# Optimization experiments

Measured on AMD Instinct MI355X. Metric: run time of the kernel, lower is better.

Reference implementation:

```python
import jax, jax.numpy as jnp
import numpy as np

N_NODES = 100000
N_EDGES = 600000
N_GRAPHS = 4096
F_IN = 74
H = 128
L = 3
BN_EPS = 1e-5


def setup_inputs() -> dict:
    key = jax.random.key(0)
    ks = jax.random.split(key, 12)
    x = jax.random.normal(ks[0], (N_NODES, F_IN), dtype=jnp.float32)
    edge_index = jax.random.randint(ks[1], (2, N_EDGES), 0, N_NODES)
    batch = jnp.sort(jax.random.randint(ks[2], (N_NODES,), 0, N_GRAPHS))

    def lin(k, fan_in, fan_out):
        return (jax.random.normal(k, (fan_in, fan_out), dtype=jnp.float32)
                / np.float32(np.sqrt(fan_in)))

    emb_W = lin(ks[3], F_IN, H)
    emb_b = jnp.zeros((H,), jnp.float32)
    conv_W = jax.random.normal(ks[4], (L, H, H), dtype=jnp.float32) / np.float32(np.sqrt(H))
    conv_b = jnp.zeros((L, H), jnp.float32)
    bn_gamma = jnp.ones((L, H), jnp.float32)
    bn_beta = jnp.zeros((L, H), jnp.float32)
    w1 = lin(ks[5], 2 * H, H)
    b1 = jnp.zeros((H,), jnp.float32)
    w2 = lin(ks[6], H, H // 2)
    b2 = jnp.zeros((H // 2,), jnp.float32)
    w3 = lin(ks[7], H // 2, 1)
    b3 = jnp.zeros((1,), jnp.float32)
    return dict(x=x, edge_index=edge_index, batch=batch,
                emb_W=emb_W, emb_b=emb_b, conv_W=conv_W, conv_b=conv_b,
                bn_gamma=bn_gamma, bn_beta=bn_beta,
                w1=w1, b1=b1, w2=w2, b2=b2, w3=w3, b3=b3)


def reference(x, edge_index, batch, emb_W, emb_b, conv_W, conv_b,
              bn_gamma, bn_beta, w1, b1, w2, b2, w3, b3):
    N = x.shape[0]
    # GCN normalization with self-loops (PyG GCNConv semantics)
    loops = jnp.arange(N)
    src = jnp.concatenate([edge_index[0], loops])  # [E+N]
    dst = jnp.concatenate([edge_index[1], loops])
    deg = jax.ops.segment_sum(jnp.ones_like(dst, jnp.float32), dst, num_segments=N)
    dinv = jax.lax.rsqrt(jnp.maximum(deg, 1.0))  # deg >= 1 due to self-loops
    norm = dinv[src] * dinv[dst]                 # [E+N]

    h = jax.nn.relu(x @ emb_W + emb_b)           # [N, H]
    for i in range(L):
        hw = h @ conv_W[i]                       # [N, H]
        msg = hw[src] * norm[:, None]            # gather + scale  [E+N, H]
        h = jax.ops.segment_sum(msg, dst, num_segments=N) + conv_b[i]
        # BatchNorm1d, training-mode batch statistics (biased variance)
        mu = jnp.mean(h, axis=0)
        var = jnp.mean((h - mu) ** 2, axis=0)
        h = (h - mu) * jax.lax.rsqrt(var + BN_EPS) * bn_gamma[i] + bn_beta[i]
        h = jax.nn.relu(h)
        # dropout: identity (inference / deterministic baseline)

    # segment mean / max pooling over graphs
    cnt = jax.ops.segment_sum(jnp.ones((N,), jnp.float32), batch, num_segments=N_GRAPHS)
    g_mean = jax.ops.segment_sum(h, batch, num_segments=N_GRAPHS) / jnp.maximum(cnt, 1.0)[:, None]
    g_max = jax.ops.segment_max(h, batch, num_segments=N_GRAPHS)
    g_max = jnp.where(jnp.isfinite(g_max), g_max, 0.0)  # guard empty segments
    g = jnp.concatenate([g_mean, g_max], axis=1)         # [G, 2H]

    h1 = jax.nn.relu(g @ w1 + b1)
    h2 = jax.nn.relu(h1 @ w2 + b2)
    return h2 @ w3 + b3                                   # [G, 1]
```

## Files before the change

### kernel.cpp

```cpp
#include <hip/hip_runtime.h>

#define NN 100000
#define NE 600000
#define NG 4096
#define FIN 74
#define HD 128
#define NL 3
#define BN_EPS 1e-5f
#define NSCAN 391
#define NHISTB 2344
#define NT16 6250
#define NSHADOW 8

typedef __attribute__((ext_vector_type(8))) short short8;
typedef __attribute__((ext_vector_type(4))) float floatx4;
typedef __attribute__((ext_vector_type(8))) unsigned short bf16x8;
typedef __attribute__((ext_vector_type(4))) unsigned short bf16x4;

__device__ __forceinline__ unsigned short f2bf(float f) {
    unsigned u = __float_as_uint(f);
    u += 0x7fff + ((u >> 16) & 1);
    return (unsigned short)(u >> 16);
}
__device__ __forceinline__ float bf2f(unsigned short u) {
    return __uint_as_float(((unsigned)u) << 16);
}

__global__ __launch_bounds__(256) void k_pre(const int* __restrict__ dst,
                                             int* __restrict__ degi,
                                             const int* __restrict__ batch,
                                             int* __restrict__ gstart,
                                             const float* __restrict__ embW,
                                             const float* __restrict__ convW,
                                             unsigned short* __restrict__ WfE,
                                             unsigned short* __restrict__ WfC) {
    int blk = blockIdx.x;
    int t = threadIdx.x;
    if (blk < NHISTB) {
        int e = blk * 256 + t;
        if (e < NE) atomicAdd(&degi[dst[e]], 1);
    } else if (blk < NHISTB + NSCAN) {
        int n = (blk - NHISTB) * 256 + t;
        if (n >= NN) return;
        int b = batch[n];
        int bp = (n == 0) ? -1 : batch[n - 1];
        for (int g = bp + 1; g <= b; g++) gstart[g] = n;
        if (n == NN - 1)
            for (int g = b + 1; g <= NG; g++) gstart[g] = NN;
    } else {
        int d = (blk - NHISTB - NSCAN) * 256 + t;
        if (d < 12288) {
            int inner = d & 511, outer = d >> 9;
            int kstep = outer % 3, nt = outer / 3;
            int g = inner >> 7, n = (inner >> 3) & 15, j = inner & 7;
            int k = kstep * 32 + g * 8 + j;
            float v = (k < FIN) ? embW[k * HD + nt * 16 + n] : 0.0f;
            WfE[d] = f2bf(v);
        } else {
            int e = d - 12288;
            if (e >= NL * 16384) return;
            int layer = e >> 14, r = e & 16383;
            int j = r & 7, n = (r >> 3) & 15, g = (r >> 7) & 3, kstep = (r >> 9) & 3, nt = r >> 11;
            int k = kstep * 32 + g * 8 + j;
            WfC[e] = f2bf(convW[layer * 16384 + k * HD + nt * 16 + n]);
        }
    }
}

__global__ __launch_bounds__(256) void k_scan1(const int* __restrict__ degi,
                                               int* __restrict__ part) {
    __shared__ int s[256];
    int t = threadIdx.x;
    int idx = blockIdx.x * 256 + t;
    s[t] = (idx < NN) ? degi[idx] : 0;
    __syncthreads();
    for (int off = 128; off > 0; off >>= 1) {
        if (t < off) s[t] += s[t + off];
        __syncthreads();
    }
    if (t == 0) part[blockIdx.x] = s[0];
}

__global__ __launch_bounds__(512) void k_scan2(int* __restrict__ part) {
    __shared__ int s[512];
    int t = threadIdx.x;
    s[t] = (t < NSCAN) ? part[t] : 0;
    __syncthreads();
    for (int off = 1; off < 512; off <<= 1) {
        int v = s[t];
        int a = (t >= off) ? s[t - off] : 0;
        __syncthreads();
        s[t] = v + a;
        __syncthreads();
    }
    if (t < NSCAN) part[t] = (t > 0) ? s[t - 1] : 0;
}

__global__ __launch_bounds__(256) void k_scan3(const int* __restrict__ degi,
                                               const int* __restrict__ part,
                                               int* __restrict__ rowptr,
                                               float* __restrict__ dinv) {
    __shared__ int s[256];
    int t = threadIdx.x;
    int idx = blockIdx.x * 256 + t;
    int v = (idx < NN) ? degi[idx] : 0;
    s[t] = v;
    __syncthreads();
    for (int off = 1; off < 256; off <<= 1) {
        int x = s[t];
        int a = (t >= off) ? s[t - off] : 0;
        __syncthreads();
        s[t] = x + a;
        __syncthreads();
    }
    if (idx < NN) {
        rowptr[idx] = part[blockIdx.x] + (s[t] - v);
        dinv[idx] = rsqrtf((float)v + 1.0f);
    }
    if (idx == 0) rowptr[NN] = NE;
}

__global__ __launch_bounds__(256) void k_fill(const int* __restrict__ src,
                                              const int* __restrict__ dst,
                                              const int* __restrict__ rowptr,
                                              int* __restrict__ cursor,
                                              int* __restrict__ col) {
    int e = blockIdx.x * 256 + threadIdx.x;
    if (e >= NE) return;
    int d = dst[e];
    int pos = rowptr[d] + atomicAdd(&cursor[d], 1);
    col[pos] = src[e];
}

__global__ __launch_bounds__(256) void k_emb(const float* __restrict__ x,
                                             const unsigned short* __restrict__ Wf,
                                             const float* __restrict__ b,
                                             const float* __restrict__ dinv,
                                             unsigned short* __restrict__ hA) {
    __shared__ __align__(16) unsigned short As[4224];
    __shared__ float dinvs[32];
    int t = threadIdx.x;
    int n0 = blockIdx.x * 32;
    if (t < 32) dinvs[t] = dinv[n0 + t];
    for (int f = t; f < 3072; f += 256) {
        int m = f / 96, kp = f % 96;
        float v = (kp < FIN) ? x[(n0 + m) * FIN + kp] : 0.0f;
        int kstep = kp >> 5, g = (kp >> 3) & 3, j = kp & 7;
        As[(kstep * 4 + g) * 264 + m * 8 + j] = f2bf(v);
    }
    __syncthreads();
    int lane = t & 63, wv = t >> 6;
    int lanelo = lane & 15, g = lane >> 4;
    floatx4 acc[2][2] = {};
#pragma unroll
    for (int kstep = 0; kstep < 3; kstep++) {
        short8 a0 = *(const short8*)&As[(kstep * 4 + g) * 264 + lanelo * 8];
        short8 a1 = *(const short8*)&As[(kstep * 4 + g) * 264 + 128 + lanelo * 8];
        short8 b0 = *(const short8*)&Wf[(((wv * 2 + 0) * 3 + kstep) * 4 + g) * 128 + lanelo * 8];
        short8 b1 = *(const short8*)&Wf[(((wv * 2 + 1) * 3 + kstep) * 4 + g) * 128 + lanelo * 8];
        acc[0][0] = __builtin_amdgcn_mfma_f32_16x16x32_bf16(a0, b0, acc[0][0], 0, 0, 0);
        acc[0][1] = __builtin_amdgcn_mfma_f32_16x16x32_bf16(a0, b1, acc[0][1], 0, 0, 0);
        acc[1][0] = __builtin_amdgcn_mfma_f32_16x16x32_bf16(a1, b0, acc[1][0], 0, 0, 0);
        acc[1][1] = __builtin_amdgcn_mfma_f32_16x16x32_bf16(a1, b1, acc[1][1], 0, 0, 0);
    }
    __syncthreads();
#pragma unroll
    for (int ns = 0; ns < 2; ns++) {
        int colc = wv * 32 + ns * 16 + lanelo;
        float bias = b[colc];
#pragma unroll
        for (int ms = 0; ms < 2; ms++)
#pragma unroll
            for (int r = 0; r < 4; r++) {
                int rowl = ms * 16 + g * 4 + r;
                As[rowl * 132 + colc] = f2bf(dinvs[rowl] * fmaxf(acc[ms][ns][r] + bias, 0.0f));
            }
    }
    __syncthreads();
#pragma unroll
    for (int i = 0; i < 2; i++) {
        int f = t * 8 + i * 2048;
        int m = f >> 7, c = f & 127;
        bf16x4 lo = *(const bf16x4*)&As[m * 132 + c];
        bf16x4 hi = *(const bf16x4*)&As[m * 132 + c + 4];
        bf16x8 o = {lo.x, lo.y, lo.z, lo.w, hi.x, hi.y, hi.z, hi.w};
        *(bf16x8*)&hA[n0 * HD + f] = o;
    }
}

__global__ __launch_bounds__(256) void k_bnact(const unsigned short* __restrict__ hpre,
                                               const float* __restrict__ bnsum,
                                               const float* __restrict__ gamma,
                                               const float* __restrict__ beta,
                                               const float* __restrict__ dinv,
                                               unsigned short* __restrict__ P) {
    int t = threadIdx.x;
    int cg = t & 15, c0 = cg * 8;
    const float inv_n = 1.0f / (float)NN;
    float sc[8], sh[8];
#pragma unroll
    for (int jj = 0; jj < 8; jj++) {
        int c = c0 + jj;
        float s = 0.0f, q = 0.0f;
#pragma unroll
        for (int kk = 0; kk < NSHADOW; kk++) {
            s += bnsum[kk * 256 + c];
            q += bnsum[kk * 256 + 128 + c];
        }
        float mu = s * inv_n;
        float var = q * inv_n - mu * mu;
        float g = gamma[c] * rsqrtf(var + BN_EPS);
        sc[jj] = g;
        sh[jj] = beta[c] - mu * g;
    }
    for (int n = blockIdx.x * 16 + (t >> 4); n < NN; n += gridDim.x * 16) {
        float d = dinv[n];
        bf16x8 u = *(const bf16x8*)&hpre[n * HD + c0];
        bf16x8 o;
#pragma unroll
        for (int i = 0; i < 8; i++)
            o[i] = f2bf(d * fmaxf(bf2f(u[i]) * sc[i] + sh[i], 0.0f));
        *(bf16x8*)&P[n * HD + c0] = o;
    }
}

__global__ __launch_bounds__(256, 8) void k_fused(const unsigned short* __restrict__ Ain,
                                                  const int* __restrict__ rowptr,
                                                  const int* __restrict__ col,
                                                  const float* __restrict__ dinv,
                                                  const unsigned short* __restrict__ Wf,
                                                  const float* __restrict__ bias,
                                                  float* __restrict__ bnout,
                                                  unsigned short* __restrict__ Aout) {
    __shared__ __align__(16) unsigned short As[2176];
    int t = threadIdx.x;
    int slot = t >> 4;
    int lanec = t & 15;
    int k0 = lanec * 8;

    int lane = t & 63, wv = t >> 6;
    int lanelo = lane & 15, g = lane >> 4;
    float bias0 = bias[wv * 32 + lanelo];
    float bias1 = bias[wv * 32 + 16 + lanelo];
    float ssum[2] = {}, ssq[2] = {};

    int n0 = blockIdx.x * 16;
    {
        int n = n0 + slot;
        float dn = dinv[n];
        float acc[8];
        bf16x8 u = *(const bf16x8*)&Ain[n * HD + k0];
#pragma unroll
        for (int i = 0; i < 8; i++) acc[i] = bf2f(u[i]);
        int j = rowptr[n], j1 = rowptr[n + 1];
        for (; j + 3 < j1; j += 4) {
            int s0 = col[j], s1 = col[j + 1], s2 = col[j + 2], s3 = col[j + 3];
            bf16x8 v0 = *(const bf16x8*)&Ain[s0 * HD + k0];
            bf16x8 v1 = *(const bf16x8*)&Ain[s1 * HD + k0];
            bf16x8 v2 = *(const bf16x8*)&Ain[s2 * HD + k0];
            bf16x8 v3 = *(const bf16x8*)&Ain[s3 * HD + k0];
#pragma unroll
            for (int i = 0; i < 8; i++) {
                float a01 = bf2f(v0[i]) + bf2f(v1[i]);
                float a23 = bf2f(v2[i]) + bf2f(v3[i]);
                acc[i] += a01 + a23;
            }
        }
        for (; j < j1; j++) {
            int s0 = col[j];
            bf16x8 v0 = *(const bf16x8*)&Ain[s0 * HD + k0];
#pragma unroll
            for (int i = 0; i < 8; i++) acc[i] += bf2f(v0[i]);
        }
        bf16x8 o;
#pragma unroll
        for (int i = 0; i < 8; i++) o[i] = f2bf(acc[i] * dn);
        *(bf16x8*)&As[lanec * 136 + slot * 8] = o;
    }
    __syncthreads();
    floatx4 macc[2] = {};
#pragma unroll
    for (int ks = 0; ks < 4; ks++) {
        short8 a = *(const short8*)&As[(ks * 4 + g) * 136 + lanelo * 8];
        short8 b0 = *(const short8*)&Wf[(((wv * 2 + 0) * 4 + ks) * 4 + g) * 128 + lanelo * 8];
        short8 b1 = *(const short8*)&Wf[(((wv * 2 + 1) * 4 + ks) * 4 + g) * 128 + lanelo * 8];
        macc[0] = __builtin_amdgcn_mfma_f32_16x16x32_bf16(a, b0, macc[0], 0, 0, 0);
        macc[1] = __builtin_amdgcn_mfma_f32_16x16x32_bf16(a, b1, macc[1], 0, 0, 0);
    }
    __syncthreads();
#pragma unroll
    for (int ns = 0; ns < 2; ns++) {
        int colc = wv * 32 + ns * 16 + lanelo;
        float bb = ns ? bias1 : bias0;
#pragma unroll
        for (int r = 0; r < 4; r++) {
            int rowl = g * 4 + r;
            float v = macc[ns][r] + bb;
            ssum[ns] += v;
            ssq[ns] += v * v;
            As[rowl * 132 + colc] = f2bf(v);
        }
    }
    __syncthreads();
    {
        int m = t >> 4, c = (t & 15) * 8;
        bf16x4 lo = *(const bf16x4*)&As[m * 132 + c];
        bf16x4 hi = *(const bf16x4*)&As[m * 132 + c + 4];
        bf16x8 o = {lo.x, lo.y, lo.z, lo.w, hi.x, hi.y, hi.z, hi.w};
        *(bf16x8*)&Aout[n0 * HD + t * 8] = o;
    }
    __syncthreads();
    float* ls = (float*)As;
    ls[t] = 0.0f;
    __syncthreads();
    {
        int colc0 = wv * 32 + lanelo;
        atomicAdd(&ls[colc0], ssum[0]);
        atomicAdd(&ls[128 + colc0], ssq[0]);
        atomicAdd(&ls[colc0 + 16], ssum[1]);
        atomicAdd(&ls[128 + colc0 + 16], ssq[1]);
    }
    __syncthreads();
    atomicAdd(&bnout[(blockIdx.x & (NSHADOW - 1)) * 256 + t], ls[t]);
}

__global__ __launch_bounds__(128) void k_pool_g(const unsigned short* __restrict__ h,
                                                const float* __restrict__ bnsum,
                                                const float* __restrict__ gamma,
                                                const float* __restrict__ beta,
                                                const int* __restrict__ gstart,
                                                float* __restrict__ gfeat) {
    int g = blockIdx.x;
    int c = threadIdx.x;
    int n0 = gstart[g], n1 = gstart[g + 1];
    const float inv_n = 1.0f / (float)NN;
    float s0 = 0.0f, q0 = 0.0f;
#pragma unroll
    for (int k = 0; k < NSHADOW; k++) {
        s0 += bnsum[k * 256 + c];
        q0 += bnsum[k * 256 + 128 + c];
    }
    float mu = s0 * inv_n;
    float var = q0 * inv_n - mu * mu;
    float sc = gamma[c] * rsqrtf(var + BN_EPS);
    float sh = beta[c] - mu * sc;
    float s = 0.0f, mx = 0.0f;
    for (int n = n0; n < n1; n++) {
        float v = fmaxf(bf2f(h[n * HD + c]) * sc + sh, 0.0f);
        s += v;
        mx = fmaxf(mx, v);
    }
    float cntf = (float)(n1 - n0);
    gfeat[g * 256 + c] = s / fmaxf(cntf, 1.0f);
    gfeat[g * 256 + HD + c] = mx;
}

__global__ __launch_bounds__(256) void k_mlp(const float* __restrict__ gfeat,
                                             const float* __restrict__ w1,
                                             const float* __restrict__ b1,
                                             const float* __restrict__ w2,
                                             const float* __restrict__ b2,
                                             const float* __restrict__ w3,
                                             const float* __restrict__ b3,
                                             float* __restrict__ out) {
    __shared__ float gs[8][258];
    __shared__ float p1[8][130];
    __shared__ float hs[8][130];
    __shared__ float p2[3][8][66];
    __shared__ float h2s[8][66];
    __shared__ float ps[64];
    int t = threadIdx.x;
    int g0 = blockIdx.x * 8;
    for (int f = t; f < 2048; f += 256) {
        int gi = f >> 8, k = f & 255;
        gs[gi][k] = gfeat[(g0 + gi) * 256 + k];
    }
    __syncthreads();
    {
        int colc = t & 127, half = t >> 7;
        int kb = half * 128;
        float acc[8] = {};
        for (int k = 0; k < 128; k++) {
            float w = w1[(kb + k) * HD + colc];
#pragma unroll
            for (int gi = 0; gi < 8; gi++) acc[gi] += gs[gi][kb + k] * w;
        }
        if (half == 1) {
#pragma unroll
            for (int gi = 0; gi < 8; gi++) p1[gi][colc] = acc[gi];
        }
        __syncthreads();
        if (half == 0) {
            float bias = b1[colc];
#pragma unroll
            for (int gi = 0; gi < 8; gi++)
                hs[gi][colc] = fmaxf(acc[gi] + p1[gi][colc] + bias, 0.0f);
        }
    }
    __syncthreads();
    {
        int colc = t & 63, q = t >> 6;
        int kb = q * 32;
        float acc[8] = {};
        for (int k = 0; k < 32; k++) {
            float w = w2[(kb + k) * 64 + colc];
#pragma unroll
            for (int gi = 0; gi < 8; gi++) acc[gi] += hs[gi][kb + k] * w;
        }
        if (q > 0) {
#pragma unroll
            for (int gi = 0; gi < 8; gi++) p2[q - 1][gi][colc] = acc[gi];
        }
        __syncthreads();
        if (q == 0) {
            float bias = b2[colc];
#pragma unroll
            for (int gi = 0; gi < 8; gi++)
                h2s[gi][colc] = fmaxf(acc[gi] + p2[0][gi][colc] + p2[1][gi][colc]
                                      + p2[2][gi][colc] + bias, 0.0f);
        }
    }
    __syncthreads();
    if (t < 64) {
        int gi = t >> 3, prt = t & 7;
        float p = 0.0f;
#pragma unroll
        for (int k = 0; k < 8; k++) p += h2s[gi][prt * 8 + k] * w3[prt * 8 + k];
        ps[t] = p;
    }
    __syncthreads();
    if (t < 8) {
        float a = b3[0];
#pragma unroll
        for (int i = 0; i < 8; i++) a += ps[t * 8 + i];
        out[g0 + t] = a;
    }
}

extern "C" void kernel_launch(void* const* d_in, const int* in_sizes, int n_in,
                              void* d_out, int out_size, void* d_ws, size_t ws_size,
                              hipStream_t stream) {
    const float* x      = (const float*)d_in[0];
    const int*   eidx   = (const int*)d_in[1];
    const int*   batch  = (const int*)d_in[2];
    const float* emb_W  = (const float*)d_in[3];
    const float* emb_b  = (const float*)d_in[4];
    const float* conv_W = (const float*)d_in[5];
    const float* conv_b = (const float*)d_in[6];
    const float* gamma  = (const float*)d_in[7];
    const float* beta   = (const float*)d_in[8];
    const float* w1     = (const float*)d_in[9];
    const float* b1     = (const float*)d_in[10];
    const float* w2     = (const float*)d_in[11];
    const float* b2     = (const float*)d_in[12];
    const float* w3     = (const float*)d_in[13];
    const float* b3     = (const float*)d_in[14];
    float* out = (float*)d_out;

    const int* src = eidx;
    const int* dst = eidx + NE;

    unsigned short* A = (unsigned short*)d_ws;
    unsigned short* B = A + NN * HD;
    float* dinv  = (float*)(B + NN * HD);
    float* gfeat = dinv + NN;
    float* bnsum3= gfeat + NG * 256;
    int*   degi  = (int*)(bnsum3 + NL * NSHADOW * 256);
    int*   cursor= degi + NN;
    int*   gstart= cursor + NN;
    int*   rowptr= gstart + NG + 1;
    int*   part  = rowptr + NN + 1;
    int*   col   = part + NSCAN;
    unsigned short* WfE = (unsigned short*)(col + NE);
    unsigned short* WfC = WfE + 12288;

    (void)hipMemsetAsync(bnsum3, 0,
                         (NL * NSHADOW * 256) * sizeof(float) + 2 * NN * sizeof(int),
                         stream);
    k_pre<<<NHISTB + NSCAN + 240, 256, 0, stream>>>(dst, degi, batch, gstart,
                                                    emb_W, conv_W, WfE, WfC);
    k_scan1<<<NSCAN, 256, 0, stream>>>(degi, part);
    k_scan2<<<1, 512, 0, stream>>>(part);
    k_scan3<<<NSCAN, 256, 0, stream>>>(degi, part, rowptr, dinv);
    k_fill<<<(NE + 255) / 256, 256, 0, stream>>>(src, dst, rowptr, cursor, col);

    k_emb<<<NN / 32, 256, 0, stream>>>(x, WfE, emb_b, dinv, A);

    k_fused<<<NT16, 256, 0, stream>>>(A, rowptr, col, dinv,
                                      WfC, conv_b, bnsum3, B);
    k_bnact<<<1024, 256, 0, stream>>>(B, bnsum3, gamma, beta, dinv, A);
    k_fused<<<NT16, 256, 0, stream>>>(A, rowptr, col, dinv,
                                      WfC + 16384, conv_b + HD,
                                      bnsum3 + NSHADOW * 256, B);
    k_bnact<<<1024, 256, 0, stream>>>(B, bnsum3 + NSHADOW * 256,
                                      gamma + HD, beta + HD, dinv, A);
    k_fused<<<NT16, 256, 0, stream>>>(A, rowptr, col, dinv,
                                      WfC + 2 * 16384, conv_b + 2 * HD,
                                      bnsum3 + 2 * NSHADOW * 256, B);

    k_pool_g<<<NG, 128, 0, stream>>>(B, bnsum3 + 2 * NSHADOW * 256,
                                     gamma + 2 * HD, beta + 2 * HD,
                                     gstart, gfeat);

    k_mlp<<<NG / 8, 256, 0, stream>>>(gfeat, w1, b1, w2, b2, w3, b3, out);
}
```

Before: 382.8 us.

## Double tile to 32 nodes per block and software-pipeline neighbor gathers

The fused aggregate+GEMM kernel now processes 32 nodes per 512-thread block. Its eight waves split into two row blocks times four column pairs, which halves the grid and the per-block BN-statistics global atomics. The neighbor gather loop is software-pipelined: the next four neighbor rows are loaded before the current four are accumulated, to hide gather latency. The cost is more registers per thread under a tighter launch bound (512 threads, 8 blocks), which risks spills or lower occupancy.

```diff
diff --git a/kernel.cpp b/kernel.cpp
--- a/kernel.cpp
+++ b/kernel.cpp
@@ -9,7 +9,7 @@
 #define BN_EPS 1e-5f
 #define NSCAN 391
 #define NHISTB 2344
-#define NT16 6250
+#define NTILES 3125
 #define NSHADOW 8
 
 typedef __attribute__((ext_vector_type(8))) short short8;
@@ -224,7 +224,7 @@
     }
 }
 
-__global__ __launch_bounds__(256, 8) void k_fused(const unsigned short* __restrict__ Ain,
+__global__ __launch_bounds__(512, 8) void k_fused(const unsigned short* __restrict__ Ain,
                                                   const int* __restrict__ rowptr,
                                                   const int* __restrict__ col,
                                                   const float* __restrict__ dinv,
@@ -232,19 +232,21 @@
                                                   const float* __restrict__ bias,
                                                   float* __restrict__ bnout,
                                                   unsigned short* __restrict__ Aout) {
-    __shared__ __align__(16) unsigned short As[2176];
+    __shared__ __align__(16) unsigned short As[4224];
     int t = threadIdx.x;
     int slot = t >> 4;
     int lanec = t & 15;
     int k0 = lanec * 8;
 
-    int lane = t & 63, wv = t >> 6;
-    int lanelo = lane & 15, g = lane >> 4;
-    float bias0 = bias[wv * 32 + lanelo];
-    float bias1 = bias[wv * 32 + 16 + lanelo];
+    int wv = t >> 6;
+    int lanelo = t & 15, g = (t & 63) >> 4;
+    int rowblk = wv >> 2;
+    int colpair = wv & 3;
+    float bias0 = bias[colpair * 32 + lanelo];
+    float bias1 = bias[colpair * 32 + 16 + lanelo];
     float ssum[2] = {}, ssq[2] = {};
 
-    int n0 = blockIdx.x * 16;
+    int n0 = blockIdx.x * 32;
     {
         int n = n0 + slot;
         float dn = dinv[n];
@@ -253,48 +255,66 @@
 #pragma unroll
         for (int i = 0; i < 8; i++) acc[i] = bf2f(u[i]);
         int j = rowptr[n], j1 = rowptr[n + 1];
-        for (; j + 3 < j1; j += 4) {
+        bf16x8 v0 = {}, v1 = {}, v2 = {}, v3 = {};
+        if (j + 3 < j1) {
             int s0 = col[j], s1 = col[j + 1], s2 = col[j + 2], s3 = col[j + 3];
-            bf16x8 v0 = *(const bf16x8*)&Ain[s0 * HD + k0];
-            bf16x8 v1 = *(const bf16x8*)&Ain[s1 * HD + k0];
-            bf16x8 v2 = *(const bf16x8*)&Ain[s2 * HD + k0];
-            bf16x8 v3 = *(const bf16x8*)&Ain[s3 * HD + k0];
+            v0 = *(const bf16x8*)&Ain[s0 * HD + k0];
+            v1 = *(const bf16x8*)&Ain[s1 * HD + k0];
+            v2 = *(const bf16x8*)&Ain[s2 * HD + k0];
+            v3 = *(const bf16x8*)&Ain[s3 * HD + k0];
+        }
+        for (; j + 7 < j1; j += 4) {
+            int s4 = col[j + 4], s5 = col[j + 5], s6 = col[j + 6], s7 = col[j + 7];
+            bf16x8 w0 = *(const bf16x8*)&Ain[s4 * HD + k0];
+            bf16x8 w1 = *(const bf16x8*)&Ain[s5 * HD + k0];
+            bf16x8 w2 = *(const bf16x8*)&Ain[s6 * HD + k0];
+            bf16x8 w3 = *(const bf16x8*)&Ain[s7 * HD + k0];
 #pragma unroll
             for (int i = 0; i < 8; i++) {
                 float a01 = bf2f(v0[i]) + bf2f(v1[i]);
                 float a23 = bf2f(v2[i]) + bf2f(v3[i]);
                 acc[i] += a01 + a23;
             }
+            v0 = w0; v1 = w1; v2 = w2; v3 = w3;
+        }
+        if (j + 3 < j1) {
+#pragma unroll
+            for (int i = 0; i < 8; i++) {
+                float a01 = bf2f(v0[i]) + bf2f(v1[i]);
+                float a23 = bf2f(v2[i]) + bf2f(v3[i]);
+                acc[i] += a01 + a23;
+            }
+            j += 4;
         }
         for (; j < j1; j++) {
             int s0 = col[j];
-            bf16x8 v0 = *(const bf16x8*)&Ain[s0 * HD + k0];
-#pragma unroll
-            for (int i = 0; i < 8; i++) acc[i] += bf2f(v0[i]);
+            bf16x8 vv = *(const bf16x8*)&Ain[s0 * HD + k0];
+#pragma unroll
+            for (int i = 0; i < 8; i++) acc[i] += bf2f(vv[i]);
         }
         bf16x8 o;
 #pragma unroll
         for (int i = 0; i < 8; i++) o[i] = f2bf(acc[i] * dn);
-        *(bf16x8*)&As[lanec * 136 + slot * 8] = o;
+        *(bf16x8*)&As[lanec * 264 + slot * 8] = o;
     }
     __syncthreads();
     floatx4 macc[2] = {};
 #pragma unroll
     for (int ks = 0; ks < 4; ks++) {
-        short8 a = *(const short8*)&As[(ks * 4 + g) * 136 + lanelo * 8];
-        short8 b0 = *(const short8*)&Wf[(((wv * 2 + 0) * 4 + ks) * 4 + g) * 128 + lanelo * 8];
-        short8 b1 = *(const short8*)&Wf[(((wv * 2 + 1) * 4 + ks) * 4 + g) * 128 + lanelo * 8];
+        short8 a = *(const short8*)&As[(ks * 4 + g) * 264 + rowblk * 128 + lanelo * 8];
+        short8 b0 = *(const short8*)&Wf[(((colpair * 2 + 0) * 4 + ks) * 4 + g) * 128 + lanelo * 8];
+        short8 b1 = *(const short8*)&Wf[(((colpair * 2 + 1) * 4 + ks) * 4 + g) * 128 + lanelo * 8];
         macc[0] = __builtin_amdgcn_mfma_f32_16x16x32_bf16(a, b0, macc[0], 0, 0, 0);
         macc[1] = __builtin_amdgcn_mfma_f32_16x16x32_bf16(a, b1, macc[1], 0, 0, 0);
     }
     __syncthreads();
 #pragma unroll
     for (int ns = 0; ns < 2; ns++) {
-        int colc = wv * 32 + ns * 16 + lanelo;
+        int colc = colpair * 32 + ns * 16 + lanelo;
         float bb = ns ? bias1 : bias0;
 #pragma unroll
         for (int r = 0; r < 4; r++) {
-            int rowl = g * 4 + r;
+            int rowl = rowblk * 16 + g * 4 + r;
             float v = macc[ns][r] + bb;
             ssum[ns] += v;
             ssq[ns] += v * v;
@@ -311,17 +331,17 @@
     }
     __syncthreads();
     float* ls = (float*)As;
-    ls[t] = 0.0f;
+    if (t < 256) ls[t] = 0.0f;
     __syncthreads();
     {
-        int colc0 = wv * 32 + lanelo;
+        int colc0 = colpair * 32 + lanelo;
         atomicAdd(&ls[colc0], ssum[0]);
         atomicAdd(&ls[128 + colc0], ssq[0]);
         atomicAdd(&ls[colc0 + 16], ssum[1]);
         atomicAdd(&ls[128 + colc0 + 16], ssq[1]);
     }
     __syncthreads();
-    atomicAdd(&bnout[(blockIdx.x & (NSHADOW - 1)) * 256 + t], ls[t]);
+    if (t < 256) atomicAdd(&bnout[(blockIdx.x & (NSHADOW - 1)) * 256 + t], ls[t]);
 }
 
 __global__ __launch_bounds__(128) void k_pool_g(const unsigned short* __restrict__ h,
@@ -486,17 +506,17 @@
 
     k_emb<<<NN / 32, 256, 0, stream>>>(x, WfE, emb_b, dinv, A);
 
-    k_fused<<<NT16, 256, 0, stream>>>(A, rowptr, col, dinv,
-                                      WfC, conv_b, bnsum3, B);
+    k_fused<<<NTILES, 512, 0, stream>>>(A, rowptr, col, dinv,
+                                        WfC, conv_b, bnsum3, B);
     k_bnact<<<1024, 256, 0, stream>>>(B, bnsum3, gamma, beta, dinv, A);
-    k_fused<<<NT16, 256, 0, stream>>>(A, rowptr, col, dinv,
-                                      WfC + 16384, conv_b + HD,
-                                      bnsum3 + NSHADOW * 256, B);
+    k_fused<<<NTILES, 512, 0, stream>>>(A, rowptr, col, dinv,
+                                        WfC + 16384, conv_b + HD,
+                                        bnsum3 + NSHADOW * 256, B);
     k_bnact<<<1024, 256, 0, stream>>>(B, bnsum3 + NSHADOW * 256,
                                       gamma + HD, beta + HD, dinv, A);
-    k_fused<<<NT16, 256, 0, stream>>>(A, rowptr, col, dinv,
-                                      WfC + 2 * 16384, conv_b + 2 * HD,
-                                      bnsum3 + 2 * NSHADOW * 256, B);
+    k_fused<<<NTILES, 512, 0, stream>>>(A, rowptr, col, dinv,
+                                        WfC + 2 * 16384, conv_b + 2 * HD,
+                                        bnsum3 + 2 * NSHADOW * 256, B);
 
     k_pool_g<<<NG, 128, 0, stream>>>(B, bnsum3 + 2 * NSHADOW * 256,
                                      gamma + 2 * HD, beta + 2 * HD,
```

Measured after the change: 389.0 us. About the same (+1.6%).
